# Kernel optimization log

Measured on AMD Instinct MI355X. Metric: run time of the kernel, lower is better.

## Reference

```python
import jax, jax.numpy as jnp
import numpy as np

DIM, N_HEADS, N_EXPERTS, TOP_K = 1024, 16, 8, 2
D_FF = 4 * DIM
HEAD_DIM = DIM // N_HEADS
EPS = 1e-5


def layer_norm(x, g, b):
    m = x.mean(-1, keepdims=True)
    v = ((x - m) ** 2).mean(-1, keepdims=True)
    return (x - m) / jnp.sqrt(v + EPS) * g + b


def setup_inputs() -> dict:
    key = jax.random.key(0)
    ks = jax.random.split(key, 16)
    B, T = 8, 1024
    s = 0.02
    inp = {
        'x': jax.random.normal(ks[0], (B, T, DIM), jnp.float32),
        'attention_mask': jnp.ones((B, T), jnp.int32),
        'Wq': jax.random.normal(ks[1], (DIM, DIM), jnp.float32) * s,
        'bq': jnp.zeros((DIM,), jnp.float32),
        'Wk': jax.random.normal(ks[2], (DIM, DIM), jnp.float32) * s,
        'bk': jnp.zeros((DIM,), jnp.float32),
        'Wv': jax.random.normal(ks[3], (DIM, DIM), jnp.float32) * s,
        'bv': jnp.zeros((DIM,), jnp.float32),
        'Wo': jax.random.normal(ks[4], (DIM, DIM), jnp.float32) * s,
        'bo': jnp.zeros((DIM,), jnp.float32),
        'g1': jnp.ones((DIM,), jnp.float32),
        'beta1': jnp.zeros((DIM,), jnp.float32),
        'router_w': jax.random.normal(ks[5], (DIM, N_EXPERTS), jnp.float32) * s,
        'router_b': jnp.zeros((N_EXPERTS,), jnp.float32),
        'W1': jax.random.normal(ks[6], (N_EXPERTS, DIM, D_FF), jnp.float32) * s,
        'B1': jnp.zeros((N_EXPERTS, D_FF), jnp.float32),
        'W2': jax.random.normal(ks[7], (N_EXPERTS, D_FF, DIM), jnp.float32) * s,
        'B2': jnp.zeros((N_EXPERTS, DIM), jnp.float32),
        'g2': jnp.ones((DIM,), jnp.float32),
        'beta2': jnp.zeros((DIM,), jnp.float32),
    }
    return inp


def reference(x, attention_mask, Wq, bq, Wk, bk, Wv, bv, Wo, bo, g1, beta1,
              router_w, router_b, W1, B1, W2, B2, g2, beta2):
    B, T, D = x.shape
    H, hd = N_HEADS, HEAD_DIM
    # ---- multi-head attention with causal + padding mask ----
    q = (x @ Wq + bq).reshape(B, T, H, hd).transpose(0, 2, 1, 3)  # [B,H,T,hd]
    k = (x @ Wk + bk).reshape(B, T, H, hd).transpose(0, 2, 1, 3)
    v = (x @ Wv + bv).reshape(B, T, H, hd).transpose(0, 2, 1, 3)
    scores = jnp.einsum('bhqd,bhkd->bhqk', q, k) / jnp.sqrt(jnp.float32(hd))
    causal = jnp.tril(jnp.ones((T, T), bool))[None, None]            # [1,1,T,T]
    mask = causal & (attention_mask[:, None, None, :] != 0)         # [B,1,T,T]
    scores = jnp.where(mask, scores, jnp.float32(-1e9))
    attn = jax.nn.softmax(scores, axis=-1)
    h = jnp.einsum('bhqk,bhkd->bhqd', attn, v).transpose(0, 2, 1, 3).reshape(B, T, D)
    h = h @ Wo + bo
    # dropout is identity in eval mode
    x1 = layer_norm(x + h, g1, beta1)
    # ---- sparse top-k MoE FFN ----
    xf = x1.reshape(-1, D)                                           # [N,D]
    logits = xf @ router_w + router_b                                # [N,E]
    probs = jax.nn.softmax(logits, axis=-1)
    topv, topi = jax.lax.top_k(probs, TOP_K)                         # [N,k]
    gk = topv / topv.sum(-1, keepdims=True)                          # renormalized gates
    onehot = jax.nn.one_hot(topi, N_EXPERTS, dtype=xf.dtype)         # [N,k,E]
    gates = (onehot * gk[..., None]).sum(1)                          # [N,E]
    y = jnp.zeros_like(xf)
    for e in range(N_EXPERTS):  # fixed small expert loop
        he = jax.nn.relu(xf @ W1[e] + B1[e])
        y = y + gates[:, e:e + 1] * (he @ W2[e] + B2[e])
    # load-balancing loss: E * sum_i f_i * P_i
    f = onehot.sum(1).mean(0)                                        # fraction routed per expert
    P = probs.mean(0)
    lb = jnp.float32(N_EXPERTS) * (f * P).sum()
    out = layer_norm(x1 + y.reshape(B, T, D), g2, beta2)
    return out, lb
```

## Files before the change

kernel.cpp:

```cpp
#include <hip/hip_runtime.h>
#include <hip/hip_bf16.h>
#include <stdint.h>

#define DIMQ   1024
#define NHEADS 16
#define HD     64
#define NEXP   8
#define DFF    4096
#define NTOK   8192
#define TSEQ   1024
#define BATCH  8

typedef unsigned short u16;
typedef unsigned int   u32;
typedef __attribute__((ext_vector_type(8))) short bf16x8;
typedef __attribute__((ext_vector_type(4))) float f32x4;

__device__ __forceinline__ float bf_lo(u32 w) { return __uint_as_float(w << 16); }
__device__ __forceinline__ float bf_hi(u32 w) { return __uint_as_float(w & 0xffff0000u); }
__device__ __forceinline__ u16 f2bf(float f) {
  u32 x = __float_as_uint(f);
  return (u16)((x + 0x7fffu + ((x >> 16) & 1u)) >> 16);
}

__device__ __forceinline__ void gload16(const u16* g, u16* l) {
  __builtin_amdgcn_global_load_lds((const __attribute__((address_space(1))) u32*)g,
                                   (__attribute__((address_space(3))) u32*)l, 16, 0, 0);
}

__global__ __launch_bounds__(256) void cvt_f32_bf16(const float* __restrict__ in,
                                                    u16* __restrict__ out, int n) {
  int i = (blockIdx.x * 256 + threadIdx.x) * 4;
  if (i >= n) return;
  float4 v = *(const float4*)(in + i);
  ushort4 o;
  o.x = f2bf(v.x); o.y = f2bf(v.y); o.z = f2bf(v.z); o.w = f2bf(v.w);
  *(ushort4*)(out + i) = o;
}

__global__ __launch_bounds__(256) void transpose_f32_bf16(
    const float* __restrict__ in, u16* __restrict__ out, int R, int C) {
  __shared__ float tile[32][33];
  size_t base = (size_t)blockIdx.z * (size_t)R * (size_t)C;
  int tx = threadIdx.x & 31, ty = threadIdx.x >> 5;
  int c = blockIdx.x * 32 + tx;
#pragma unroll
  for (int i = 0; i < 4; i++) {
    int r = blockIdx.y * 32 + ty + i * 8;
    tile[ty + i * 8][tx] = in[base + (size_t)r * C + c];
  }
  __syncthreads();
  int rr = blockIdx.y * 32 + tx;
#pragma unroll
  for (int i = 0; i < 4; i++) {
    int cc = blockIdx.x * 32 + ty + i * 8;
    out[base + (size_t)cc * R + rr] = f2bf(tile[tx][ty + i * 8]);
  }
}

template <bool GATHER, bool RELU, bool TRANSC>
__device__ __forceinline__ void gemm_core(
    const u16* __restrict__ A, const u16* __restrict__ Bt,
    const float* __restrict__ bias, u16* __restrict__ C,
    int M, int N, int K, const int* __restrict__ gidx) {
  __shared__ u16 As[128 * 32];
  __shared__ u16 Bs[128 * 32];
  const int tid = threadIdx.x;
  const int lane = tid & 63;
  const int wave = tid >> 6;
  const int wr = wave >> 1, wc = wave & 1;
  const int lr = lane & 15, kg = lane >> 4;
  const int rowbase = blockIdx.y * 128;
  const int colbase = blockIdx.x * 128;

  f32x4 acc[4][4];
#pragma unroll
  for (int m = 0; m < 4; m++)
#pragma unroll
    for (int n = 0; n < 4; n++) acc[m][n] = (f32x4){0.f, 0.f, 0.f, 0.f};

  const int r0 = tid >> 2, seg = tid & 3;
  const int slog = seg ^ ((r0 >> 1) & 3);
  int ar0 = rowbase + r0;      if (ar0 >= M) ar0 = M - 1;
  int ar1 = rowbase + r0 + 64; if (ar1 >= M) ar1 = M - 1;
  const long arow0 = GATHER ? gidx[ar0] : ar0;
  const long arow1 = GATHER ? gidx[ar1] : ar1;
  const u16* Aptr0 = A + (size_t)arow0 * K + slog * 8;
  const u16* Aptr1 = A + (size_t)arow1 * K + slog * 8;
  const u16* Bptr0 = Bt + (size_t)(colbase + r0) * K + slog * 8;
  const u16* Bptr1 = Bt + (size_t)(colbase + r0 + 64) * K + slog * 8;
  u16* ldsA0 = &As[tid * 8];
  u16* ldsA1 = &As[2048 + tid * 8];
  u16* ldsB0 = &Bs[tid * 8];
  u16* ldsB1 = &Bs[2048 + tid * 8];

  const int swz = (lr >> 1) & 3;

  for (int k0 = 0; k0 < K; k0 += 32) {
    gload16(Aptr0 + k0, ldsA0);
    gload16(Aptr1 + k0, ldsA1);
    gload16(Bptr0 + k0, ldsB0);
    gload16(Bptr1 + k0, ldsB1);
    __syncthreads();
    bf16x8 af[4], bfr[4];
#pragma unroll
    for (int m = 0; m < 4; m++)
      af[m] = *(const bf16x8*)(&As[(wr * 64 + m * 16 + lr) * 32 + ((kg ^ swz) * 8)]);
#pragma unroll
    for (int n = 0; n < 4; n++)
      bfr[n] = *(const bf16x8*)(&Bs[(wc * 64 + n * 16 + lr) * 32 + ((kg ^ swz) * 8)]);
#pragma unroll
    for (int m = 0; m < 4; m++)
#pragma unroll
      for (int n = 0; n < 4; n++)
        acc[m][n] = __builtin_amdgcn_mfma_f32_16x16x32_bf16(af[m], bfr[n], acc[m][n], 0, 0, 0);
    __syncthreads();
  }
#pragma unroll
  for (int n = 0; n < 4; n++) {
    int col = colbase + wc * 64 + n * 16 + lr;
    float bv = bias[col];
#pragma unroll
    for (int m = 0; m < 4; m++) {
      int row0 = rowbase + wr * 64 + m * 16 + kg * 4;
      if (TRANSC) {
        if (row0 + 3 < M) {
          ushort4 pk;
          pk.x = f2bf(acc[m][n][0] + bv);
          pk.y = f2bf(acc[m][n][1] + bv);
          pk.z = f2bf(acc[m][n][2] + bv);
          pk.w = f2bf(acc[m][n][3] + bv);
          *(ushort4*)(&C[(size_t)col * M + row0]) = pk;
        } else {
#pragma unroll
          for (int r = 0; r < 4; r++)
            if (row0 + r < M) C[(size_t)col * M + row0 + r] = f2bf(acc[m][n][r] + bv);
        }
      } else {
#pragma unroll
        for (int r = 0; r < 4; r++) {
          int row = row0 + r;
          if (row < M) {
            float v = acc[m][n][r] + bv;
            if (RELU) v = fmaxf(v, 0.f);
            C[(size_t)row * N + col] = f2bf(v);
          }
        }
      }
    }
  }
}

__global__ __launch_bounds__(256) void gemm_bt_kernel(
    const u16* __restrict__ A, const u16* __restrict__ Bt,
    const float* __restrict__ bias, u16* __restrict__ C, int M, int N, int K) {
  gemm_core<false, false, false>(A, Bt, bias, C, M, N, K, nullptr);
}

__global__ __launch_bounds__(256) void gemm_bt_tc_kernel(
    const u16* __restrict__ A, const u16* __restrict__ Bt,
    const float* __restrict__ bias, u16* __restrict__ C, int M, int N, int K) {
  gemm_core<false, false, true>(A, Bt, bias, C, M, N, K, nullptr);
}

template <bool GATHER, bool RELU>
__device__ __forceinline__ void gemm256_core(
    const u16* __restrict__ A, const u16* __restrict__ Bt,
    const float* __restrict__ bias, u16* __restrict__ C,
    int M, int N, int K, const int* __restrict__ gidx) {
  __shared__ u16 lds[2][2][256 * 64];
  const int tid = threadIdx.x;
  const int lane = tid & 63;
  const int wave = tid >> 6;
  const int wr = wave >> 2;
  const int wcol = wave & 3;
  const int lr = lane & 15, kg = lane >> 4;
  const int rowbase = blockIdx.y * 256;
  const int colbase = blockIdx.x * 256;

  f32x4 acc[8][4];
#pragma unroll
  for (int m = 0; m < 8; m++)
#pragma unroll
    for (int n = 0; n < 4; n++) acc[m][n] = (f32x4){0.f, 0.f, 0.f, 0.f};

  const int srow0 = tid >> 3, sphys = tid & 7;
  const u16* asrc[4];
  const u16* bsrc[4];
#pragma unroll
  for (int j = 0; j < 4; j++) {
    int row = srow0 + j * 64;
    int ls = sphys ^ (row & 7);
    int ar = rowbase + row; if (ar >= M) ar = M - 1;
    long ga = GATHER ? gidx[ar] : ar;
    asrc[j] = A + (size_t)ga * K + ls * 8;
    bsrc[j] = Bt + (size_t)(colbase + row) * K + ls * 8;
  }

#define STAGE256(buf, k0)                                              \
  {                                                                    \
    _Pragma("unroll")                                                  \
    for (int j = 0; j < 4; j++) {                                      \
      gload16(asrc[j] + (k0), &lds[buf][0][tid * 8 + j * 4096]);       \
      gload16(bsrc[j] + (k0), &lds[buf][1][tid * 8 + j * 4096]);       \
    }                                                                  \
  }

  STAGE256(0, 0);
  __syncthreads();
  const int NT = K >> 6;
  for (int t = 0; t < NT; t++) {
    const int buf = t & 1;
    if (t + 1 < NT) STAGE256(buf ^ 1, (t + 1) << 6);
    bf16x8 bfr[4][2];
#pragma unroll
    for (int nr = 0; nr < 4; nr++) {
      int rb = wcol * 64 + nr * 16 + lr;
#pragma unroll
      for (int kk = 0; kk < 2; kk++)
        bfr[nr][kk] = *(const bf16x8*)(&lds[buf][1][rb * 64 + (((kk * 4 + kg) ^ (rb & 7)) * 8)]);
    }
#pragma unroll
    for (int mr = 0; mr < 8; mr++) {
      int ra = wr * 128 + mr * 16 + lr;
      bf16x8 a0 = *(const bf16x8*)(&lds[buf][0][ra * 64 + ((kg ^ (ra & 7)) * 8)]);
      bf16x8 a1 = *(const bf16x8*)(&lds[buf][0][ra * 64 + (((4 + kg) ^ (ra & 7)) * 8)]);
#pragma unroll
      for (int nr = 0; nr < 4; nr++) {
        acc[mr][nr] = __builtin_amdgcn_mfma_f32_16x16x32_bf16(a0, bfr[nr][0], acc[mr][nr], 0, 0, 0);
        acc[mr][nr] = __builtin_amdgcn_mfma_f32_16x16x32_bf16(a1, bfr[nr][1], acc[mr][nr], 0, 0, 0);
      }
    }
    __syncthreads();
  }
#undef STAGE256

#pragma unroll
  for (int nr = 0; nr < 4; nr++) {
    int col = colbase + wcol * 64 + nr * 16 + lr;
    float bv = bias[col];
#pragma unroll
    for (int mr = 0; mr < 8; mr++) {
      int row0 = rowbase + wr * 128 + mr * 16 + kg * 4;
#pragma unroll
      for (int r = 0; r < 4; r++) {
        int row = row0 + r;
        if (row < M) {
          float v = acc[mr][nr][r] + bv;
          if (RELU) v = fmaxf(v, 0.f);
          C[(size_t)row * N + col] = f2bf(v);
        }
      }
    }
  }
}

__global__ __launch_bounds__(512, 2) void moe_gemm1_kernel(
    const u16* __restrict__ x1b, const u16* __restrict__ W1t,
    const float* __restrict__ B1, u16* __restrict__ he,
    const int* __restrict__ cnt, const int* __restrict__ off,
    const int* __restrict__ idxlist) {
  int e = blockIdx.z;
  int M = cnt[e];
  if ((int)blockIdx.y * 256 >= M) return;
  gemm256_core<true, true>(x1b, W1t + (size_t)e * DFF * DIMQ, B1 + e * DFF,
                           he + (size_t)off[e] * DFF, M, DFF, DIMQ, idxlist + off[e]);
}

__global__ __launch_bounds__(512, 2) void moe_gemm2_kernel(
    const u16* __restrict__ he, const u16* __restrict__ W2t,
    const float* __restrict__ B2, u16* __restrict__ yslot,
    const int* __restrict__ cnt, const int* __restrict__ off) {
  int e = blockIdx.z;
  int M = cnt[e];
  if ((int)blockIdx.y * 256 >= M) return;
  gemm256_core<false, false>(he + (size_t)off[e] * DFF, W2t + (size_t)e * DIMQ * DFF,
                             B2 + e * DIMQ, yslot + (size_t)off[e] * DIMQ, M, DIMQ, DFF, nullptr);
}

__global__ __launch_bounds__(256) void attn_mfma_kernel(
    const u16* __restrict__ qb, const u16* __restrict__ kb,
    const u16* __restrict__ vbT, const int* __restrict__ amask,
    u16* __restrict__ hb) {
  __shared__ u16 Ks[32 * 64];
  __shared__ u16 VTs[64 * 32];
  __shared__ u16 Ps[4][16 * 32];
  __shared__ float mbias[32];

  const int b = blockIdx.y >> 4;
  const int h = blockIdx.y & 15;
  const int qb0 = blockIdx.x * 64;
  const int tid = threadIdx.x;
  const int lane = tid & 63;
  const int wq = tid >> 6;
  const int r16 = lane & 15;
  const int kg = lane >> 4;
  const int qrow0 = qb0 + wq * 16;

  bf16x8 qf[2];
  {
    const u16* qp = qb + ((size_t)(b * TSEQ + qrow0 + r16)) * DIMQ + h * HD + kg * 8;
    qf[0] = *(const bf16x8*)(qp);
    qf[1] = *(const bf16x8*)(qp + 32);
  }
  f32x4 acc[4];
#pragma unroll
  for (int db = 0; db < 4; db++) acc[db] = (f32x4){0.f, 0.f, 0.f, 0.f};
  float m_run[4], l_run[4];
#pragma unroll
  for (int i = 0; i < 4; i++) { m_run[i] = -3.0e38f; l_run[i] = 0.f; }

  const int skey = tid >> 3, sslot = tid & 7;
  const int sd = tid >> 2, sko = tid & 3;
  const u16* kgb = kb + (size_t)(b * TSEQ) * DIMQ + h * HD;
  const u16* vgb = vbT + (size_t)(h * HD) * NTOK + (size_t)b * TSEQ;

  const int nt = (qb0 + 64) >> 5;
  for (int kt = 0; kt < nt; kt++) {
    const int k0g = kt * 32;
    __syncthreads();
    {
      uint4 kv = *(const uint4*)(kgb + (size_t)(k0g + skey) * DIMQ + sslot * 8);
      *(uint4*)(&Ks[skey * 64 + ((sslot ^ (skey & 7)) * 8)]) = kv;
      uint4 vv = *(const uint4*)(vgb + (size_t)sd * NTOK + k0g + sko * 8);
      *(uint4*)(&VTs[sd * 32 + ((sko ^ (sd & 3)) * 8)]) = vv;
      if (tid < 32) mbias[tid] = amask[b * TSEQ + k0g + tid] ? 0.f : -1e9f;
    }
    __syncthreads();
    if (k0g < qrow0 + 16) {
      f32x4 s0 = (f32x4){0.f, 0.f, 0.f, 0.f};
      f32x4 s1 = (f32x4){0.f, 0.f, 0.f, 0.f};
      {
        int key0 = r16;
        bf16x8 ka = *(const bf16x8*)(&Ks[key0 * 64 + ((kg ^ (key0 & 7)) * 8)]);
        bf16x8 kb2 = *(const bf16x8*)(&Ks[key0 * 64 + (((4 + kg) ^ (key0 & 7)) * 8)]);
        s0 = __builtin_amdgcn_mfma_f32_16x16x32_bf16(qf[0], ka, s0, 0, 0, 0);
        s0 = __builtin_amdgcn_mfma_f32_16x16x32_bf16(qf[1], kb2, s0, 0, 0, 0);
        int key1 = 16 + r16;
        bf16x8 kc = *(const bf16x8*)(&Ks[key1 * 64 + ((kg ^ (key1 & 7)) * 8)]);
        bf16x8 kd = *(const bf16x8*)(&Ks[key1 * 64 + (((4 + kg) ^ (key1 & 7)) * 8)]);
        s1 = __builtin_amdgcn_mfma_f32_16x16x32_bf16(qf[0], kc, s1, 0, 0, 0);
        s1 = __builtin_amdgcn_mfma_f32_16x16x32_bf16(qf[1], kd, s1, 0, 0, 0);
      }
      float sv0[4], sv1[4], tm[4];
      float mb0 = mbias[r16], mb1 = mbias[16 + r16];
#pragma unroll
      for (int i = 0; i < 4; i++) {
        int qg = qrow0 + kg * 4 + i;
        float a = s0[i] * 0.125f + mb0;
        float c = s1[i] * 0.125f + mb1;
        if (k0g + r16 > qg)      a = -3.0e38f;
        if (k0g + 16 + r16 > qg) c = -3.0e38f;
        sv0[i] = a; sv1[i] = c;
        tm[i] = fmaxf(a, c);
      }
#pragma unroll
      for (int mk = 1; mk < 16; mk <<= 1) {
#pragma unroll
        for (int i = 0; i < 4; i++) tm[i] = fmaxf(tm[i], __shfl_xor(tm[i], mk));
      }
      float pr0[4], pr1[4];
#pragma unroll
      for (int i = 0; i < 4; i++) {
        float nm = fmaxf(m_run[i], tm[i]);
        float sc = __expf(m_run[i] - nm);
        m_run[i] = nm;
        pr0[i] = __expf(sv0[i] - nm);
        pr1[i] = __expf(sv1[i] - nm);
        l_run[i] = l_run[i] * sc + pr0[i] + pr1[i];
#pragma unroll
        for (int db = 0; db < 4; db++) acc[db][i] *= sc;
      }
#pragma unroll
      for (int i = 0; i < 4; i++) {
        int qrl = kg * 4 + i;
        int sw = qrl & 3;
        Ps[wq][qrl * 32 + (((r16 >> 3) ^ sw) * 8) + (r16 & 7)] = f2bf(pr0[i]);
        Ps[wq][qrl * 32 + ((((16 + r16) >> 3) ^ sw) * 8) + (r16 & 7)] = f2bf(pr1[i]);
      }
      bf16x8 pf = *(const bf16x8*)(&Ps[wq][r16 * 32 + ((kg ^ (r16 & 3)) * 8)]);
#pragma unroll
      for (int db = 0; db < 4; db++) {
        int d = db * 16 + r16;
        bf16x8 vf = *(const bf16x8*)(&VTs[d * 32 + ((kg ^ (d & 3)) * 8)]);
        acc[db] = __builtin_amdgcn_mfma_f32_16x16x32_bf16(pf, vf, acc[db], 0, 0, 0);
      }
    }
  }
#pragma unroll
  for (int mk = 1; mk < 16; mk <<= 1) {
#pragma unroll
    for (int i = 0; i < 4; i++) l_run[i] += __shfl_xor(l_run[i], mk);
  }
#pragma unroll
  for (int i = 0; i < 4; i++) {
    float inv = 1.f / l_run[i];
    int qg = qrow0 + kg * 4 + i;
    u16* op = hb + ((size_t)(b * TSEQ + qg)) * DIMQ + h * HD + r16;
#pragma unroll
    for (int db = 0; db < 4; db++) op[db * 16] = f2bf(acc[db][i] * inv);
  }
}

__global__ __launch_bounds__(256) void addln_kernel(
    const float* __restrict__ xin, const u16* __restrict__ hres,
    const float* __restrict__ g, const float* __restrict__ beta,
    float* __restrict__ x1, u16* __restrict__ x1b) {
  __shared__ float red[8];
  int t = blockIdx.x;
  int d = threadIdx.x * 4;
  size_t base = (size_t)t * DIMQ + d;
  float4 xv = *(const float4*)(xin + base);
  uint2 hu = *(const uint2*)(hres + base);
  float v0 = xv.x + bf_lo(hu.x), v1 = xv.y + bf_hi(hu.x);
  float v2 = xv.z + bf_lo(hu.y), v3 = xv.w + bf_hi(hu.y);
  float s1 = v0 + v1 + v2 + v3;
  float s2 = v0 * v0 + v1 * v1 + v2 * v2 + v3 * v3;
#pragma unroll
  for (int off = 32; off; off >>= 1) {
    s1 += __shfl_down(s1, off);
    s2 += __shfl_down(s2, off);
  }
  int w = threadIdx.x >> 6;
  if ((threadIdx.x & 63) == 0) { red[w] = s1; red[4 + w] = s2; }
  __syncthreads();
  float S1 = red[0] + red[1] + red[2] + red[3];
  float S2 = red[4] + red[5] + red[6] + red[7];
  float m = S1 * (1.f / DIMQ);
  float var = S2 * (1.f / DIMQ) - m * m;
  float rs = rsqrtf(var + 1e-5f);
  float4 gv = *(const float4*)(g + d);
  float4 bv = *(const float4*)(beta + d);
  float o0 = (v0 - m) * rs * gv.x + bv.x;
  float o1 = (v1 - m) * rs * gv.y + bv.y;
  float o2 = (v2 - m) * rs * gv.z + bv.z;
  float o3 = (v3 - m) * rs * gv.w + bv.w;
  *(float4*)(x1 + base) = make_float4(o0, o1, o2, o3);
  uint2 pu;
  pu.x = (u32)f2bf(o0) | ((u32)f2bf(o1) << 16);
  pu.y = (u32)f2bf(o2) | ((u32)f2bf(o3) << 16);
  *(uint2*)(x1b + base) = pu;
}

__global__ __launch_bounds__(256) void router_kernel(
    const float* __restrict__ x1, const float* __restrict__ rw,
    const float* __restrict__ rb, int* __restrict__ topi,
    float* __restrict__ gkout, float* __restrict__ probs) {
  int t = blockIdx.x * 4 + (threadIdx.x >> 6);
  int l = threadIdx.x & 63;
  float acc[8];
#pragma unroll
  for (int e = 0; e < 8; e++) acc[e] = 0.f;
  const float* xr = x1 + (size_t)t * DIMQ;
  for (int k = l; k < DIMQ; k += 64) {
    float xv = xr[k];
    const float* w = rw + (size_t)k * 8;
#pragma unroll
    for (int e = 0; e < 8; e++) acc[e] += xv * w[e];
  }
#pragma unroll
  for (int e = 0; e < 8; e++) {
#pragma unroll
    for (int off = 32; off; off >>= 1) acc[e] += __shfl_down(acc[e], off);
  }
  if (l == 0) {
    float lg[8], p[8];
    float mx = -3e38f;
#pragma unroll
    for (int e = 0; e < 8; e++) { lg[e] = acc[e] + rb[e]; mx = fmaxf(mx, lg[e]); }
    float sum = 0.f;
#pragma unroll
    for (int e = 0; e < 8; e++) { p[e] = expf(lg[e] - mx); sum += p[e]; }
    float isum = 1.f / sum;
#pragma unroll
    for (int e = 0; e < 8; e++) p[e] *= isum;
    int e0 = 0;
#pragma unroll
    for (int e = 1; e < 8; e++) if (p[e] > p[e0]) e0 = e;
    int e1 = (e0 == 0) ? 1 : 0;
#pragma unroll
    for (int e = 0; e < 8; e++) if (e != e0 && p[e] > p[e1]) e1 = e;
    float s2 = p[e0] + p[e1];
    topi[2 * t] = e0; topi[2 * t + 1] = e1;
    gkout[2 * t] = p[e0] / s2; gkout[2 * t + 1] = p[e1] / s2;
    float* pp = probs + (size_t)t * 8;
#pragma unroll
    for (int e = 0; e < 8; e++) pp[e] = p[e];
  }
}

__global__ __launch_bounds__(256) void stats_kernel(
    const float* __restrict__ probs, const int* __restrict__ topi,
    int* __restrict__ cnt, float* __restrict__ Psum) {
  __shared__ float sps[4][8];
  __shared__ int   slc[4][8];
  float ps[8];
  int lc[8];
#pragma unroll
  for (int e = 0; e < 8; e++) { ps[e] = 0.f; lc[e] = 0; }
  int t = blockIdx.x * 256 + threadIdx.x;
  {
    const float* p = probs + (size_t)t * 8;
#pragma unroll
    for (int e = 0; e < 8; e++) ps[e] += p[e];
    lc[topi[2 * t]]++;
    lc[topi[2 * t + 1]]++;
  }
#pragma unroll
  for (int e = 0; e < 8; e++) {
#pragma unroll
    for (int off = 32; off; off >>= 1) {
      ps[e] += __shfl_down(ps[e], off);
      lc[e] += __shfl_down(lc[e], off);
    }
  }
  int w = threadIdx.x >> 6;
  if ((threadIdx.x & 63) == 0) {
#pragma unroll
    for (int e = 0; e < 8; e++) { sps[w][e] = ps[e]; slc[w][e] = lc[e]; }
  }
  __syncthreads();
  if (threadIdx.x < 8) {
    float fp = sps[0][threadIdx.x] + sps[1][threadIdx.x] + sps[2][threadIdx.x] + sps[3][threadIdx.x];
    int   fc = slc[0][threadIdx.x] + slc[1][threadIdx.x] + slc[2][threadIdx.x] + slc[3][threadIdx.x];
    atomicAdd(&Psum[threadIdx.x], fp);
    atomicAdd(&cnt[threadIdx.x], fc);
  }
}

__global__ void offsets_kernel(const int* __restrict__ cnt, const float* __restrict__ Psum,
                               int* __restrict__ off, int* __restrict__ fill,
                               float* __restrict__ lb_out) {
  if (threadIdx.x == 0 && blockIdx.x == 0) {
    int o = 0;
    float lb = 0.f;
    for (int e = 0; e < NEXP; e++) {
      off[e] = o;
      fill[e] = o;
      o += cnt[e];
      lb += ((float)cnt[e] / (float)NTOK) * (Psum[e] / (float)NTOK);
    }
    lb_out[0] = (float)NEXP * lb;
  }
}

__global__ __launch_bounds__(256) void listbuild_kernel(
    const int* __restrict__ topi, int* fill, int* __restrict__ idxlist,
    int* __restrict__ posmap) {
  __shared__ int bcnt[8];
  __shared__ int base[8];
  __shared__ int bofs[8];
  int t = blockIdx.x * 256 + threadIdx.x;
  if (threadIdx.x < 8) { bcnt[threadIdx.x] = 0; bofs[threadIdx.x] = 0; }
  __syncthreads();
  int e0 = topi[2 * t], e1 = topi[2 * t + 1];
  atomicAdd(&bcnt[e0], 1);
  atomicAdd(&bcnt[e1], 1);
  __syncthreads();
  if (threadIdx.x < 8) base[threadIdx.x] = atomicAdd(&fill[threadIdx.x], bcnt[threadIdx.x]);
  __syncthreads();
  int s0 = base[e0] + atomicAdd(&bofs[e0], 1);
  idxlist[s0] = t;
  posmap[2 * t] = s0;
  int s1 = base[e1] + atomicAdd(&bofs[e1], 1);
  idxlist[s1] = t;
  posmap[2 * t + 1] = s1;
}

__global__ __launch_bounds__(256) void finalln_kernel(
    const float* __restrict__ x1, const u16* __restrict__ yslot,
    const int* __restrict__ posmap, const float* __restrict__ gkv,
    const float* __restrict__ g, const float* __restrict__ beta,
    float* __restrict__ out) {
  __shared__ float red[8];
  int t = blockIdx.x;
  int p0 = posmap[2 * t], p1 = posmap[2 * t + 1];
  float g0 = gkv[2 * t], g1 = gkv[2 * t + 1];
  int d = threadIdx.x * 4;
  size_t base = (size_t)t * DIMQ + d;
  float4 xv = *(const float4*)(x1 + base);
  uint2 y0 = *(const uint2*)(yslot + (size_t)p0 * DIMQ + d);
  uint2 y1 = *(const uint2*)(yslot + (size_t)p1 * DIMQ + d);
  float v0 = xv.x + g0 * bf_lo(y0.x) + g1 * bf_lo(y1.x);
  float v1 = xv.y + g0 * bf_hi(y0.x) + g1 * bf_hi(y1.x);
  float v2 = xv.z + g0 * bf_lo(y0.y) + g1 * bf_lo(y1.y);
  float v3 = xv.w + g0 * bf_hi(y0.y) + g1 * bf_hi(y1.y);
  float s1 = v0 + v1 + v2 + v3;
  float s2 = v0 * v0 + v1 * v1 + v2 * v2 + v3 * v3;
#pragma unroll
  for (int off = 32; off; off >>= 1) {
    s1 += __shfl_down(s1, off);
    s2 += __shfl_down(s2, off);
  }
  int w = threadIdx.x >> 6;
  if ((threadIdx.x & 63) == 0) { red[w] = s1; red[4 + w] = s2; }
  __syncthreads();
  float S1 = red[0] + red[1] + red[2] + red[3];
  float S2 = red[4] + red[5] + red[6] + red[7];
  float m = S1 * (1.f / DIMQ);
  float var = S2 * (1.f / DIMQ) - m * m;
  float rs = rsqrtf(var + 1e-5f);
  float4 gv = *(const float4*)(g + d);
  float4 bv = *(const float4*)(beta + d);
  float4 o;
  o.x = (v0 - m) * rs * gv.x + bv.x;
  o.y = (v1 - m) * rs * gv.y + bv.y;
  o.z = (v2 - m) * rs * gv.z + bv.z;
  o.w = (v3 - m) * rs * gv.w + bv.w;
  *(float4*)(out + base) = o;
}

extern "C" void kernel_launch(void* const* d_in, const int* in_sizes, int n_in,
                              void* d_out, int out_size, void* d_ws, size_t ws_size,
                              hipStream_t stream) {
  const float* x     = (const float*)d_in[0];
  const int*   amask = (const int*)d_in[1];
  const float* Wq    = (const float*)d_in[2];
  const float* bq    = (const float*)d_in[3];
  const float* Wk    = (const float*)d_in[4];
  const float* bk    = (const float*)d_in[5];
  const float* Wv    = (const float*)d_in[6];
  const float* bv    = (const float*)d_in[7];
  const float* Wo    = (const float*)d_in[8];
  const float* bo    = (const float*)d_in[9];
  const float* g1    = (const float*)d_in[10];
  const float* beta1 = (const float*)d_in[11];
  const float* rw    = (const float*)d_in[12];
  const float* rb    = (const float*)d_in[13];
  const float* W1    = (const float*)d_in[14];
  const float* B1    = (const float*)d_in[15];
  const float* W2    = (const float*)d_in[16];
  const float* B2    = (const float*)d_in[17];
  const float* g2    = (const float*)d_in[18];
  const float* beta2 = (const float*)d_in[19];
  float* out    = (float*)d_out;
  float* lb_out = out + (size_t)NTOK * DIMQ;

  char* ws = (char*)d_ws;
  size_t off_acc = 0;
  auto alloc = [&](size_t bytes) {
    void* p = ws + off_acc;
    off_acc += (bytes + 255) & ~(size_t)255;
    return p;
  };
  u16* xb    = (u16*)alloc((size_t)NTOK * DIMQ * 2);
  u16* qbuf  = (u16*)alloc((size_t)NTOK * DIMQ * 2);
  u16* kbuf  = (u16*)alloc((size_t)NTOK * DIMQ * 2);
  u16* vbufT = (u16*)alloc((size_t)NTOK * DIMQ * 2);
  u16* hb    = (u16*)alloc((size_t)NTOK * DIMQ * 2);
  u16* ho    = (u16*)alloc((size_t)NTOK * DIMQ * 2);
  float* x1  = (float*)alloc((size_t)NTOK * DIMQ * 4);
  u16* x1b   = (u16*)alloc((size_t)NTOK * DIMQ * 2);
  u16* Wqt   = (u16*)alloc((size_t)DIMQ * DIMQ * 2);
  u16* Wkt   = (u16*)alloc((size_t)DIMQ * DIMQ * 2);
  u16* Wvt   = (u16*)alloc((size_t)DIMQ * DIMQ * 2);
  u16* Wot   = (u16*)alloc((size_t)DIMQ * DIMQ * 2);
  u16* W1t   = (u16*)alloc((size_t)NEXP * DFF * DIMQ * 2);
  u16* W2t   = (u16*)alloc((size_t)NEXP * DIMQ * DFF * 2);
  u16* he    = (u16*)alloc((size_t)2 * NTOK * DFF * 2);
  u16* yslot = (u16*)alloc((size_t)2 * NTOK * DIMQ * 2);
  char* stats = (char*)alloc(4096);
  int*   cnt   = (int*)stats;
  float* Psum  = (float*)(stats + 32);
  int*   offp  = (int*)(stats + 64);
  int*   fill  = (int*)(stats + 96);
  int* topi    = (int*)alloc((size_t)NTOK * 2 * 4);
  float* gkbuf = (float*)alloc((size_t)NTOK * 2 * 4);
  int* posmap  = (int*)alloc((size_t)NTOK * 2 * 4);
  int* idxlist = (int*)alloc((size_t)NTOK * 2 * 4);
  float* probs = (float*)alloc((size_t)NTOK * 8 * 4);

  hipMemsetAsync(stats, 0, 64, stream);

  cvt_f32_bf16<<<NTOK * DIMQ / 1024, 256, 0, stream>>>(x, xb, NTOK * DIMQ);
  transpose_f32_bf16<<<dim3(DIMQ / 32, DIMQ / 32, 1), 256, 0, stream>>>(Wq, Wqt, DIMQ, DIMQ);
  transpose_f32_bf16<<<dim3(DIMQ / 32, DIMQ / 32, 1), 256, 0, stream>>>(Wk, Wkt, DIMQ, DIMQ);
  transpose_f32_bf16<<<dim3(DIMQ / 32, DIMQ / 32, 1), 256, 0, stream>>>(Wv, Wvt, DIMQ, DIMQ);
  transpose_f32_bf16<<<dim3(DIMQ / 32, DIMQ / 32, 1), 256, 0, stream>>>(Wo, Wot, DIMQ, DIMQ);
  transpose_f32_bf16<<<dim3(DFF / 32, DIMQ / 32, NEXP), 256, 0, stream>>>(W1, W1t, DIMQ, DFF);
  transpose_f32_bf16<<<dim3(DIMQ / 32, DFF / 32, NEXP), 256, 0, stream>>>(W2, W2t, DFF, DIMQ);

  dim3 gproj(DIMQ / 128, NTOK / 128);
  gemm_bt_kernel<<<gproj, 256, 0, stream>>>(xb, Wqt, bq, qbuf, NTOK, DIMQ, DIMQ);
  gemm_bt_kernel<<<gproj, 256, 0, stream>>>(xb, Wkt, bk, kbuf, NTOK, DIMQ, DIMQ);
  gemm_bt_tc_kernel<<<gproj, 256, 0, stream>>>(xb, Wvt, bv, vbufT, NTOK, DIMQ, DIMQ);
  attn_mfma_kernel<<<dim3(TSEQ / 64, BATCH * NHEADS), 256, 0, stream>>>(qbuf, kbuf, vbufT, amask, hb);
  gemm_bt_kernel<<<gproj, 256, 0, stream>>>(hb, Wot, bo, ho, NTOK, DIMQ, DIMQ);
  addln_kernel<<<NTOK, 256, 0, stream>>>(x, ho, g1, beta1, x1, x1b);

  router_kernel<<<NTOK / 4, 256, 0, stream>>>(x1, rw, rb, topi, gkbuf, probs);
  stats_kernel<<<NTOK / 256, 256, 0, stream>>>(probs, topi, cnt, Psum);
  offsets_kernel<<<1, 64, 0, stream>>>(cnt, Psum, offp, fill, lb_out);
  listbuild_kernel<<<NTOK / 256, 256, 0, stream>>>(topi, fill, idxlist, posmap);
  moe_gemm1_kernel<<<dim3(DFF / 256, 32, NEXP), 512, 0, stream>>>(x1b, W1t, B1, he, cnt, offp, idxlist);
  moe_gemm2_kernel<<<dim3(DIMQ / 256, 32, NEXP), 512, 0, stream>>>(he, W2t, B2, yslot, cnt, offp);
  finalln_kernel<<<NTOK, 256, 0, stream>>>(x1, yslot, posmap, gkbuf, g2, beta2, out);
}
```

Measured before the change: 898.4 us.

## Double-buffer GEMM LDS loads with two-deep prefetch and explicit vmcnt waits

The 128-tile GEMM core moves from a single LDS buffer to double buffering, and both GEMM kernels now issue the first two stages up front. Each iteration waits only on the oldest stage's direct-to-LDS loads (explicit s_waitcnt vmcnt) plus a raw barrier, then refills the buffer just consumed with the stage two ahead. The MFMA section in the 256-tile kernel is also given raised wave priority with s_setprio. The goal is to hide global-load latency behind compute. The risks are doubled LDS use in the smaller kernel, which can lower occupancy, and correctness that depends on the hand-counted vmcnt values matching the actual number of outstanding loads.

```diff
diff --git a/kernel.cpp b/kernel.cpp
--- a/kernel.cpp
+++ b/kernel.cpp
@@ -63,8 +63,8 @@
     const u16* __restrict__ A, const u16* __restrict__ Bt,
     const float* __restrict__ bias, u16* __restrict__ C,
     int M, int N, int K, const int* __restrict__ gidx) {
-  __shared__ u16 As[128 * 32];
-  __shared__ u16 Bs[128 * 32];
+  __shared__ u16 As[2][128 * 32];
+  __shared__ u16 Bs[2][128 * 32];
   const int tid = threadIdx.x;
   const int lane = tid & 63;
   const int wave = tid >> 6;
@@ -89,33 +89,42 @@
   const u16* Aptr1 = A + (size_t)arow1 * K + slog * 8;
   const u16* Bptr0 = Bt + (size_t)(colbase + r0) * K + slog * 8;
   const u16* Bptr1 = Bt + (size_t)(colbase + r0 + 64) * K + slog * 8;
-  u16* ldsA0 = &As[tid * 8];
-  u16* ldsA1 = &As[2048 + tid * 8];
-  u16* ldsB0 = &Bs[tid * 8];
-  u16* ldsB1 = &Bs[2048 + tid * 8];
 
   const int swz = (lr >> 1) & 3;
 
-  for (int k0 = 0; k0 < K; k0 += 32) {
-    gload16(Aptr0 + k0, ldsA0);
-    gload16(Aptr1 + k0, ldsA1);
-    gload16(Bptr0 + k0, ldsB0);
-    gload16(Bptr1 + k0, ldsB1);
-    __syncthreads();
+#define STAGE128(buf, k0)                                   \
+  {                                                         \
+    gload16(Aptr0 + (k0), &As[buf][tid * 8]);               \
+    gload16(Aptr1 + (k0), &As[buf][2048 + tid * 8]);        \
+    gload16(Bptr0 + (k0), &Bs[buf][tid * 8]);               \
+    gload16(Bptr1 + (k0), &Bs[buf][2048 + tid * 8]);        \
+  }
+
+  const int NT = K >> 5;
+  STAGE128(0, 0);
+  STAGE128(1, 32);
+  for (int t = 0; t < NT; t++) {
+    const int buf = t & 1;
+    if (t + 1 < NT) asm volatile("s_waitcnt vmcnt(4)" ::: "memory");
+    else            asm volatile("s_waitcnt vmcnt(0)" ::: "memory");
+    __builtin_amdgcn_s_barrier();
     bf16x8 af[4], bfr[4];
 #pragma unroll
     for (int m = 0; m < 4; m++)
-      af[m] = *(const bf16x8*)(&As[(wr * 64 + m * 16 + lr) * 32 + ((kg ^ swz) * 8)]);
+      af[m] = *(const bf16x8*)(&As[buf][(wr * 64 + m * 16 + lr) * 32 + ((kg ^ swz) * 8)]);
 #pragma unroll
     for (int n = 0; n < 4; n++)
-      bfr[n] = *(const bf16x8*)(&Bs[(wc * 64 + n * 16 + lr) * 32 + ((kg ^ swz) * 8)]);
+      bfr[n] = *(const bf16x8*)(&Bs[buf][(wc * 64 + n * 16 + lr) * 32 + ((kg ^ swz) * 8)]);
 #pragma unroll
     for (int m = 0; m < 4; m++)
 #pragma unroll
       for (int n = 0; n < 4; n++)
         acc[m][n] = __builtin_amdgcn_mfma_f32_16x16x32_bf16(af[m], bfr[n], acc[m][n], 0, 0, 0);
-    __syncthreads();
-  }
+    __builtin_amdgcn_s_barrier();
+    if (t + 2 < NT) STAGE128(buf, (t + 2) << 5);
+  }
+#undef STAGE128
+
 #pragma unroll
   for (int n = 0; n < 4; n++) {
     int col = colbase + wc * 64 + n * 16 + lr;
@@ -206,12 +215,14 @@
     }                                                                  \
   }
 
+  const int NT = K >> 6;
   STAGE256(0, 0);
-  __syncthreads();
-  const int NT = K >> 6;
+  STAGE256(1, 64);
   for (int t = 0; t < NT; t++) {
     const int buf = t & 1;
-    if (t + 1 < NT) STAGE256(buf ^ 1, (t + 1) << 6);
+    if (t + 1 < NT) asm volatile("s_waitcnt vmcnt(8)" ::: "memory");
+    else            asm volatile("s_waitcnt vmcnt(0)" ::: "memory");
+    __builtin_amdgcn_s_barrier();
     bf16x8 bfr[4][2];
 #pragma unroll
     for (int nr = 0; nr < 4; nr++) {
@@ -220,6 +231,7 @@
       for (int kk = 0; kk < 2; kk++)
         bfr[nr][kk] = *(const bf16x8*)(&lds[buf][1][rb * 64 + (((kk * 4 + kg) ^ (rb & 7)) * 8)]);
     }
+    __builtin_amdgcn_s_setprio(1);
 #pragma unroll
     for (int mr = 0; mr < 8; mr++) {
       int ra = wr * 128 + mr * 16 + lr;
@@ -231,7 +243,9 @@
         acc[mr][nr] = __builtin_amdgcn_mfma_f32_16x16x32_bf16(a1, bfr[nr][1], acc[mr][nr], 0, 0, 0);
       }
     }
-    __syncthreads();
+    __builtin_amdgcn_s_setprio(0);
+    __builtin_amdgcn_s_barrier();
+    if (t + 2 < NT) STAGE256(buf, (t + 2) << 6);
   }
 #undef STAGE256
 
```

Measured after the change: 928.8 us. 3.4% more time.
